# Performance work log

Hardware: AMD Instinct MI355X
Metric: run time of the kernel (lower is better)

Reference implementation:

```python
import jax, jax.numpy as jnp
import numpy as np

SR = 22050
N_MELS = 128
N_FFT = 2048
HOP = 512


def _mel_filterbank(sr, n_fft, n_mels):
    """librosa slaney-scale, slaney-normalized mel filterbank [n_mels, 1+n_fft//2]."""
    f_sp = 200.0 / 3
    min_log_hz = 1000.0
    min_log_mel = min_log_hz / f_sp
    logstep = np.log(6.4) / 27.0

    def hz_to_mel(f):
        f = np.asarray(f, dtype=np.float64)
        return np.where(f >= min_log_hz,
                        min_log_mel + np.log(np.maximum(f, min_log_hz) / min_log_hz) / logstep,
                        f / f_sp)

    def mel_to_hz(m):
        m = np.asarray(m, dtype=np.float64)
        return np.where(m >= min_log_mel,
                        min_log_hz * np.exp(logstep * (m - min_log_mel)),
                        f_sp * m)

    fmax = sr / 2.0
    fftfreqs = np.linspace(0.0, sr / 2.0, 1 + n_fft // 2)
    mel_f = mel_to_hz(np.linspace(hz_to_mel(0.0), hz_to_mel(fmax), n_mels + 2))
    fdiff = np.diff(mel_f)
    ramps = mel_f[:, None] - fftfreqs[None, :]
    lower = -ramps[:-2] / fdiff[:-1, None]
    upper = ramps[2:] / fdiff[1:, None]
    weights = np.maximum(0.0, np.minimum(lower, upper))
    enorm = 2.0 / (mel_f[2:n_mels + 2] - mel_f[:n_mels])  # slaney norm
    weights *= enorm[:, None]
    return weights.astype(np.float32)


def setup_inputs() -> dict:
    key = jax.random.key(0)
    x = jax.random.normal(key, (8, 661500, 2), dtype=jnp.float32) * 0.1
    mel_fb = jnp.asarray(_mel_filterbank(SR, N_FFT, N_MELS))  # [n_mels, 1+n_fft//2]
    return {"x": x, "mel_fb": mel_fb}


def reference(x, mel_fb):
    # x: (B, S, C) -> (B, n_mels, T, C), power-2 mel spectrogram (librosa defaults)
    y = jnp.transpose(x, (0, 2, 1))  # (B, C, S)
    pad = N_FFT // 2
    y = jnp.pad(y, ((0, 0), (0, 0), (pad, pad)), mode='reflect')
    n_frames = 1 + (y.shape[-1] - N_FFT) // HOP
    n = jnp.arange(N_FFT)
    # periodic hann window (scipy get_window('hann', N, fftbins=True))
    window = (0.5 - 0.5 * jnp.cos(2.0 * jnp.pi * n / N_FFT)).astype(x.dtype)
    idx = jnp.arange(n_frames)[:, None] * HOP + n[None, :]  # (T, n_fft)
    frames = y[:, :, idx] * window  # (B, C, T, n_fft)
    spec = jnp.fft.rfft(frames, axis=-1)  # (B, C, T, 1+n_fft//2)
    power = spec.real ** 2 + spec.imag ** 2  # |STFT|^2
    mel = jnp.einsum('mf,bctf->bmtc', mel_fb, power)  # (B, n_mels, T, C)
    return mel
```

## Files before the change

### kernel.cpp

```cpp
#include <hip/hip_runtime.h>
#include <math.h>

#define N_MELS   128
#define N_FFT    2048
#define HOP      512
#define BATCH    8
#define S_LEN    661500
#define CH       2
#define T_FRAMES 1292
#define NBINS    1025

#define ANG 0.003067961575771282f

#define WS_WIN     0
#define WS_TW      8192
#define WS_WBEG    24576
#define WS_WTAB    25600

#define PW_OFF   1056
#define PW_FR    2112

#define ZN 2304

__device__ __forceinline__ float2 cadd(float2 a, float2 b){ return make_float2(a.x+b.x, a.y+b.y); }
__device__ __forceinline__ float2 csub(float2 a, float2 b){ return make_float2(a.x-b.x, a.y-b.y); }
__device__ __forceinline__ float2 cmul(float2 a, float2 b){ return make_float2(a.x*b.x - a.y*b.y, a.x*b.y + a.y*b.x); }
__device__ __forceinline__ float2 cnegi(float2 z){ return make_float2(z.y, -z.x); }

__device__ __forceinline__ void bfly8(const float2* a, float2* b) {
    const float C = 0.70710678118654752f;
    float2 e0=cadd(a[0],a[4]), e1=cadd(a[1],a[5]), e2=cadd(a[2],a[6]), e3=cadd(a[3],a[7]);
    float2 o0=csub(a[0],a[4]), o1=csub(a[1],a[5]), o2=csub(a[2],a[6]), o3=csub(a[3],a[7]);
    float2 t1 = make_float2(C*(o1.x+o1.y), C*(o1.y-o1.x));
    float2 t2 = make_float2(o2.y, -o2.x);
    float2 t3 = make_float2(C*(o3.y-o3.x), -C*(o3.x+o3.y));
    {
        float2 s0=cadd(e0,e2), d0=csub(e0,e2);
        float2 s1=cadd(e1,e3), d1=csub(e1,e3);
        b[0]=cadd(s0,s1); b[4]=csub(s0,s1);
        b[2]=cadd(d0,cnegi(d1)); b[6]=csub(d0,cnegi(d1));
    }
    {
        float2 s0=cadd(o0,t2), d0=csub(o0,t2);
        float2 s1=cadd(t1,t3), d1=csub(t1,t3);
        b[1]=cadd(s0,s1); b[5]=csub(s0,s1);
        b[3]=cadd(d0,cnegi(d1)); b[7]=csub(d0,cnegi(d1));
    }
}

__device__ __forceinline__ void stage_pair(float2* rA, float2* rB, float2 w1) {
    float2 bqA[8], bqB[8];
    bfly8(rA, bqA);
    bfly8(rB, bqB);
    rA[0] = bqA[0]; rB[0] = bqB[0];
    float2 wk = w1;
    #pragma unroll
    for (int k = 1; k < 8; ++k) {
        rA[k] = cmul(wk, bqA[k]);
        rB[k] = cmul(wk, bqB[k]);
        wk = cmul(wk, w1);
    }
}

__device__ __forceinline__ void bf4(const float2* I, float2* O) {
    float2 apc=cadd(I[0],I[2]), amc=csub(I[0],I[2]);
    float2 bpd=cadd(I[1],I[3]), bmd=csub(I[1],I[3]);
    O[0]=cadd(apc,bpd); O[1]=cadd(amc,cnegi(bmd));
    O[2]=csub(apc,bpd); O[3]=csub(amc,cnegi(bmd));
}

__device__ __forceinline__ float2 upair(float2 Zf, float2 Zm) {
    float br = Zm.x, bi = -Zm.y;
    float e0 = Zf.x + br, e1 = Zf.y + bi;
    float o0 = Zf.y - bi, o1 = Zf.x - br;
    return make_float2(0.25f*(e0*e0 + e1*e1), 0.25f*(o0*o0 + o1*o1));
}

__global__ __launch_bounds__(256) void setup_kernel(
        const float* __restrict__ fb, float* __restrict__ ws) {
    int blk = blockIdx.x;
    if (blk < 8) {
        int i = blk * 256 + threadIdx.x;
        float*  win = ws;
        float2* tw  = (float2*)((char*)ws + WS_TW);
        win[i] = 0.5f - 0.5f * cosf(ANG * (float)i);
        float sn, cs; sincosf(-ANG * (float)i, &sn, &cs);
        tw[i] = make_float2(cs, sn);
    } else {
        int m = blk - 8;
        int lane = threadIdx.x;
        if (lane < 64) {
            int*   wbeg = (int*)((char*)ws + WS_WBEG);
            float* wtab = (float*)((char*)ws + WS_WTAB);
            const float* row = fb + m * NBINS;
            int s = NBINS;
            for (int f = lane; f < NBINS; f += 64)
                if (row[f] != 0.0f && f < s) s = f;
            #pragma unroll
            for (int o = 32; o; o >>= 1) s = min(s, __shfl_xor(s, o));
            int a0 = s & ~3;
            if (a0 > NBINS - 1) a0 = (NBINS - 1) & ~3;
            if (lane == 0) wbeg[m] = a0;
            int f = a0 + lane;
            wtab[(m << 6) + lane] = (f < NBINS) ? row[f] : 0.0f;
        }
    }
}

__global__ __launch_bounds__(256, 4) void mel_spec_kernel(
        const float* __restrict__ x, const float* __restrict__ fb,
        const float* __restrict__ ws, float* __restrict__ out) {
    __shared__ float4 Zq[ZN/2];
    float2* Z2  = (float2*)Zq;
    float*  pwb = (float*)Zq;

    const float*  win  = ws;
    const float2* tw   = (const float2*)((const char*)ws + WS_TW);
    const int*    wbeg = (const int*)((const char*)ws + WS_WBEG);
    const float*  wtab = (const float*)((const char*)ws + WS_WTAB);

    const int tid = threadIdx.x;
    const int bid = blockIdx.x;
    const int b   = bid & 7;
    const int t0  = (bid >> 3) * 2;

    const float2* xb = (const float2*)x + (size_t)b * S_LEN;
    const int tbA = t0*HOP - (N_FFT/2);
    const int tbB = tbA + HOP;

    float2 rA[8], rB[8];
    const int rb = tid + 2*(tid>>4);

    if (tbA >= 0 && tbB + (N_FFT - 1) < S_LEN) {
        #pragma unroll
        for (int k = 0; k < 8; ++k) {
            int n = tid + 256*k;
            float w = win[n];
            float2 vA = xb[tbA + n];
            float2 vB = xb[tbB + n];
            rA[k] = make_float2(vA.x*w, vA.y*w);
            rB[k] = make_float2(vB.x*w, vB.y*w);
        }
    } else {
        #pragma unroll
        for (int k = 0; k < 8; ++k) {
            int n  = tid + 256*k;
            float w = win[n];
            int sA = tbA + n;
            if (sA < 0) sA = -sA; else if (sA >= S_LEN) sA = 2*S_LEN - 2 - sA;
            float2 vA = xb[sA];
            rA[k] = make_float2(vA.x*w, vA.y*w);
            int sB = tbB + n;
            if (sB < 0) sB = -sB; else if (sB >= S_LEN) sB = 2*S_LEN - 2 - sB;
            float2 vB = xb[sB];
            rB[k] = make_float2(vB.x*w, vB.y*w);
        }
    }

    stage_pair(rA, rB, tw[tid]);
    {
        const int f4 = 4*tid + (tid>>1);
        #pragma unroll
        for (int j = 0; j < 4; ++j)
            Zq[f4+j] = make_float4(rA[2*j].x, rA[2*j].y, rA[2*j+1].x, rA[2*j+1].y);
        __syncthreads();
        #pragma unroll
        for (int k = 0; k < 8; ++k) rA[k] = Z2[rb + 288*k];
        __syncthreads();
        #pragma unroll
        for (int j = 0; j < 4; ++j)
            Zq[f4+j] = make_float4(rB[2*j].x, rB[2*j].y, rB[2*j+1].x, rB[2*j+1].y);
        __syncthreads();
        #pragma unroll
        for (int k = 0; k < 8; ++k) rB[k] = Z2[rb + 288*k];
        __syncthreads();
    }

    stage_pair(rA, rB, tw[tid & ~7]);
    {
        const int base = (tid & 7) + 72*(tid >> 3);
        #pragma unroll
        for (int k = 0; k < 8; ++k) Z2[base + 8*k + 2*(k>>1)] = rA[k];
        __syncthreads();
        #pragma unroll
        for (int k = 0; k < 8; ++k) rA[k] = Z2[rb + 288*k];
        __syncthreads();
        #pragma unroll
        for (int k = 0; k < 8; ++k) Z2[base + 8*k + 2*(k>>1)] = rB[k];
        __syncthreads();
        #pragma unroll
        for (int k = 0; k < 8; ++k) rB[k] = Z2[rb + 288*k];
        __syncthreads();
    }

    stage_pair(rA, rB, tw[tid & ~63]);
    const int b2  = (tid == 0) ? 256 : 512 - tid;
    const int rb2 = b2 + 2*(b2>>4);
    float2 A1[4], A2[4], B1[4], B2[4];
    {
        const int q = tid & 63;
        const int base = q + 2*(q>>4) + 576*(tid >> 6);
        #pragma unroll
        for (int k = 0; k < 8; ++k) Z2[base + 72*k] = rA[k];
        __syncthreads();
        #pragma unroll
        for (int k = 0; k < 4; ++k) { A1[k] = Z2[rb + 576*k]; A2[k] = Z2[rb2 + 576*k]; }
        __syncthreads();
        #pragma unroll
        for (int k = 0; k < 8; ++k) Z2[base + 72*k] = rB[k];
        __syncthreads();
        #pragma unroll
        for (int k = 0; k < 4; ++k) { B1[k] = Z2[rb + 576*k]; B2[k] = Z2[rb2 + 576*k]; }
        __syncthreads();
    }

    {
        float2 O1[4], O2[4];
        bf4(A1, O1); bf4(A2, O2);
        float* pwf = pwb;
        if (tid == 0) {
            float2 p;
            p = upair(O1[0], O1[0]); pwf[0]    = p.x; pwf[PW_OFF+0]    = p.y;
            p = upair(O1[1], O1[3]); pwf[512]  = p.x; pwf[PW_OFF+512]  = p.y;
            p = upair(O1[2], O1[2]); pwf[1024] = p.x; pwf[PW_OFF+1024] = p.y;
            p = upair(O2[0], O2[3]); pwf[256]  = p.x; pwf[PW_OFF+256]  = p.y;
            p = upair(O2[1], O2[2]); pwf[768]  = p.x; pwf[PW_OFF+768]  = p.y;
        } else {
            float2 p;
            p = upair(O1[0], O2[3]); pwf[tid]      = p.x; pwf[PW_OFF+tid]      = p.y;
            p = upair(O1[1], O2[2]); pwf[tid+512]  = p.x; pwf[PW_OFF+tid+512]  = p.y;
            p = upair(O2[0], O1[3]); pwf[512-tid]  = p.x; pwf[PW_OFF+512-tid]  = p.y;
            p = upair(O2[1], O1[2]); pwf[1024-tid] = p.x; pwf[PW_OFF+1024-tid] = p.y;
        }
    }
    {
        float2 O1[4], O2[4];
        bf4(B1, O1); bf4(B2, O2);
        float* pwf = pwb + PW_FR;
        if (tid == 0) {
            float2 p;
            p = upair(O1[0], O1[0]); pwf[0]    = p.x; pwf[PW_OFF+0]    = p.y;
            p = upair(O1[1], O1[3]); pwf[512]  = p.x; pwf[PW_OFF+512]  = p.y;
            p = upair(O1[2], O1[2]); pwf[1024] = p.x; pwf[PW_OFF+1024] = p.y;
            p = upair(O2[0], O2[3]); pwf[256]  = p.x; pwf[PW_OFF+256]  = p.y;
            p = upair(O2[1], O2[2]); pwf[768]  = p.x; pwf[PW_OFF+768]  = p.y;
        } else {
            float2 p;
            p = upair(O1[0], O2[3]); pwf[tid]      = p.x; pwf[PW_OFF+tid]      = p.y;
            p = upair(O1[1], O2[2]); pwf[tid+512]  = p.x; pwf[PW_OFF+tid+512]  = p.y;
            p = upair(O2[0], O1[3]); pwf[512-tid]  = p.x; pwf[PW_OFF+512-tid]  = p.y;
            p = upair(O2[1], O1[2]); pwf[1024-tid] = p.x; pwf[PW_OFF+1024-tid] = p.y;
        }
    }
    __syncthreads();

    {
        int m = tid >> 1;
        int h = tid & 1;
        int a0 = wbeg[m];
        const float4* wt4 = (const float4*)(wtab + (m << 6));
        const float*  p0  = pwb + h*PW_FR + a0;
        const float*  p1  = pwb + h*PW_FR + PW_OFF + a0;
        float acc0 = 0.0f, acc1 = 0.0f;
        #pragma unroll
        for (int j = 0; j < 16; ++j) {
            float4 w4 = wt4[j];
            float4 q0 = *(const float4*)(p0 + 4*j);
            float4 q1 = *(const float4*)(p1 + 4*j);
            acc0 += w4.x*q0.x + w4.y*q0.y + w4.z*q0.z + w4.w*q0.w;
            acc1 += w4.x*q1.x + w4.y*q1.y + w4.z*q1.z + w4.w*q1.w;
        }
        size_t base = (((size_t)b * N_MELS + m) * T_FRAMES + t0 + h) * CH;
        *(float2*)(out + base) = make_float2(acc0, acc1);
    }
}

extern "C" void kernel_launch(void* const* d_in, const int* in_sizes, int n_in,
                              void* d_out, int out_size, void* d_ws, size_t ws_size,
                              hipStream_t stream) {
    const float* x  = (const float*)d_in[0];
    const float* fb = (const float*)d_in[1];
    float* out = (float*)d_out;
    float* ws  = (float*)d_ws;

    setup_kernel<<<8 + N_MELS, 256, 0, stream>>>(fb, ws);
    mel_spec_kernel<<<BATCH * (T_FRAMES/2), 256, 0, stream>>>(x, fb, ws, out);
}
```

Before: 120.7 us.

## Process four frames per block with shared overlapping input and dual LDS buffers

Each block now computes four STFT frames instead of two. It loads one contiguous 3584-sample span once and reuses the overlapping windows across frames, instead of loading each frame separately. Two LDS buffers let the two paired FFTs transpose together, which halves the number of barriers per pair. The mel reduction reuses each weight load across four frames. The cost is double the shared memory, higher register pressure (14 input samples, four held power arrays), fewer blocks, and explicit zeroing of the padded tail of the power buffer.

```diff
diff --git a/kernel.cpp b/kernel.cpp
--- a/kernel.cpp
+++ b/kernel.cpp
@@ -17,8 +17,8 @@
 #define WS_WBEG    24576
 #define WS_WTAB    25600
 
-#define PW_OFF   1056
-#define PW_FR    2112
+#define PW_OFF   1060
+#define PW_FR    2120
 
 #define ZN 2304
 
@@ -74,6 +74,97 @@
     float e0 = Zf.x + br, e1 = Zf.y + bi;
     float o0 = Zf.y - bi, o1 = Zf.x - br;
     return make_float2(0.25f*(e0*e0 + e1*e1), 0.25f*(o0*o0 + o1*o1));
+}
+
+__device__ __forceinline__ void fft2048_pair(
+        float2* rA, float2* rB, float4* Zq0, float4* Zq1,
+        const float2* tw, int tid, int rb, int rb2,
+        float2* A1, float2* A2, float2* B1, float2* B2)
+{
+    float2* Z0 = (float2*)Zq0;
+    float2* Z1 = (float2*)Zq1;
+
+    stage_pair(rA, rB, tw[tid]);
+    {
+        const int f4 = 4*tid + (tid>>1);
+        #pragma unroll
+        for (int j = 0; j < 4; ++j) {
+            Zq0[f4+j] = make_float4(rA[2*j].x, rA[2*j].y, rA[2*j+1].x, rA[2*j+1].y);
+            Zq1[f4+j] = make_float4(rB[2*j].x, rB[2*j].y, rB[2*j+1].x, rB[2*j+1].y);
+        }
+        __syncthreads();
+        #pragma unroll
+        for (int k = 0; k < 8; ++k) { rA[k] = Z0[rb + 288*k]; rB[k] = Z1[rb + 288*k]; }
+        __syncthreads();
+    }
+
+    stage_pair(rA, rB, tw[tid & ~7]);
+    {
+        const int base = (tid & 7) + 72*(tid >> 3);
+        #pragma unroll
+        for (int k = 0; k < 8; ++k) {
+            Z0[base + 8*k + 2*(k>>1)] = rA[k];
+            Z1[base + 8*k + 2*(k>>1)] = rB[k];
+        }
+        __syncthreads();
+        #pragma unroll
+        for (int k = 0; k < 8; ++k) { rA[k] = Z0[rb + 288*k]; rB[k] = Z1[rb + 288*k]; }
+        __syncthreads();
+    }
+
+    stage_pair(rA, rB, tw[tid & ~63]);
+    {
+        const int q = tid & 63;
+        const int base = q + 2*(q>>4) + 576*(tid >> 6);
+        #pragma unroll
+        for (int k = 0; k < 8; ++k) {
+            Z0[base + 72*k] = rA[k];
+            Z1[base + 72*k] = rB[k];
+        }
+        __syncthreads();
+        #pragma unroll
+        for (int k = 0; k < 4; ++k) {
+            A1[k] = Z0[rb + 576*k]; A2[k] = Z0[rb2 + 576*k];
+            B1[k] = Z1[rb + 576*k]; B2[k] = Z1[rb2 + 576*k];
+        }
+        __syncthreads();
+    }
+}
+
+__device__ __forceinline__ void finish_frame(const float2* F1, const float2* F2,
+                                             int tid, float2* p)
+{
+    float2 O1[4], O2[4];
+    bf4(F1, O1); bf4(F2, O2);
+    if (tid == 0) {
+        p[0] = upair(O1[0], O1[0]);
+        p[1] = upair(O1[1], O1[3]);
+        p[2] = upair(O1[2], O1[2]);
+        p[3] = upair(O2[0], O2[3]);
+        p[4] = upair(O2[1], O2[2]);
+    } else {
+        p[0] = upair(O1[0], O2[3]);
+        p[1] = upair(O1[1], O2[2]);
+        p[2] = upair(O2[0], O1[3]);
+        p[3] = upair(O2[1], O1[2]);
+        p[4] = make_float2(0.0f, 0.0f);
+    }
+}
+
+__device__ __forceinline__ void store_frame(float* pwf, int tid, const float2* p)
+{
+    if (tid == 0) {
+        pwf[0]    = p[0].x; pwf[PW_OFF+0]    = p[0].y;
+        pwf[512]  = p[1].x; pwf[PW_OFF+512]  = p[1].y;
+        pwf[1024] = p[2].x; pwf[PW_OFF+1024] = p[2].y;
+        pwf[256]  = p[3].x; pwf[PW_OFF+256]  = p[3].y;
+        pwf[768]  = p[4].x; pwf[PW_OFF+768]  = p[4].y;
+    } else {
+        pwf[tid]      = p[0].x; pwf[PW_OFF+tid]      = p[0].y;
+        pwf[tid+512]  = p[1].x; pwf[PW_OFF+tid+512]  = p[1].y;
+        pwf[512-tid]  = p[2].x; pwf[PW_OFF+512-tid]  = p[2].y;
+        pwf[1024-tid] = p[3].x; pwf[PW_OFF+1024-tid] = p[3].y;
+    }
 }
 
 __global__ __launch_bounds__(256) void setup_kernel(
@@ -110,8 +201,9 @@
 __global__ __launch_bounds__(256, 4) void mel_spec_kernel(
         const float* __restrict__ x, const float* __restrict__ fb,
         const float* __restrict__ ws, float* __restrict__ out) {
-    __shared__ float4 Zq[ZN/2];
-    float2* Z2  = (float2*)Zq;
+    __shared__ float4 Zq[ZN];
+    float4* Zq0 = Zq;
+    float4* Zq1 = Zq + (ZN/2);
     float*  pwb = (float*)Zq;
 
     const float*  win  = ws;
@@ -122,156 +214,92 @@
     const int tid = threadIdx.x;
     const int bid = blockIdx.x;
     const int b   = bid & 7;
-    const int t0  = (bid >> 3) * 2;
+    const int t0  = (bid >> 3) * 4;
 
     const float2* xb = (const float2*)x + (size_t)b * S_LEN;
-    const int tbA = t0*HOP - (N_FFT/2);
-    const int tbB = tbA + HOP;
-
-    float2 rA[8], rB[8];
-    const int rb = tid + 2*(tid>>4);
-
-    if (tbA >= 0 && tbB + (N_FFT - 1) < S_LEN) {
-        #pragma unroll
-        for (int k = 0; k < 8; ++k) {
-            int n = tid + 256*k;
-            float w = win[n];
-            float2 vA = xb[tbA + n];
-            float2 vB = xb[tbB + n];
-            rA[k] = make_float2(vA.x*w, vA.y*w);
-            rB[k] = make_float2(vB.x*w, vB.y*w);
-        }
-    } else {
-        #pragma unroll
-        for (int k = 0; k < 8; ++k) {
-            int n  = tid + 256*k;
-            float w = win[n];
-            int sA = tbA + n;
-            if (sA < 0) sA = -sA; else if (sA >= S_LEN) sA = 2*S_LEN - 2 - sA;
-            float2 vA = xb[sA];
-            rA[k] = make_float2(vA.x*w, vA.y*w);
-            int sB = tbB + n;
-            if (sB < 0) sB = -sB; else if (sB >= S_LEN) sB = 2*S_LEN - 2 - sB;
-            float2 vB = xb[sB];
-            rB[k] = make_float2(vB.x*w, vB.y*w);
-        }
-    }
-
-    stage_pair(rA, rB, tw[tid]);
-    {
-        const int f4 = 4*tid + (tid>>1);
-        #pragma unroll
-        for (int j = 0; j < 4; ++j)
-            Zq[f4+j] = make_float4(rA[2*j].x, rA[2*j].y, rA[2*j+1].x, rA[2*j+1].y);
-        __syncthreads();
-        #pragma unroll
-        for (int k = 0; k < 8; ++k) rA[k] = Z2[rb + 288*k];
-        __syncthreads();
-        #pragma unroll
-        for (int j = 0; j < 4; ++j)
-            Zq[f4+j] = make_float4(rB[2*j].x, rB[2*j].y, rB[2*j+1].x, rB[2*j+1].y);
-        __syncthreads();
-        #pragma unroll
-        for (int k = 0; k < 8; ++k) rB[k] = Z2[rb + 288*k];
-        __syncthreads();
-    }
-
-    stage_pair(rA, rB, tw[tid & ~7]);
-    {
-        const int base = (tid & 7) + 72*(tid >> 3);
-        #pragma unroll
-        for (int k = 0; k < 8; ++k) Z2[base + 8*k + 2*(k>>1)] = rA[k];
-        __syncthreads();
-        #pragma unroll
-        for (int k = 0; k < 8; ++k) rA[k] = Z2[rb + 288*k];
-        __syncthreads();
-        #pragma unroll
-        for (int k = 0; k < 8; ++k) Z2[base + 8*k + 2*(k>>1)] = rB[k];
-        __syncthreads();
-        #pragma unroll
-        for (int k = 0; k < 8; ++k) rB[k] = Z2[rb + 288*k];
-        __syncthreads();
-    }
-
-    stage_pair(rA, rB, tw[tid & ~63]);
+    const int tb0 = t0*HOP - (N_FFT/2);
+
+    const int rb  = tid + 2*(tid>>4);
     const int b2  = (tid == 0) ? 256 : 512 - tid;
     const int rb2 = b2 + 2*(b2>>4);
+
+    float2 v[14];
+    float  wv[8];
+    if (tb0 >= 0 && tb0 + (3584 - 1) < S_LEN) {
+        #pragma unroll
+        for (int k = 0; k < 14; ++k) v[k] = xb[tb0 + tid + 256*k];
+    } else {
+        #pragma unroll
+        for (int k = 0; k < 14; ++k) {
+            int s = tb0 + tid + 256*k;
+            if (s < 0) s = -s; else if (s >= S_LEN) s = 2*S_LEN - 2 - s;
+            v[k] = xb[s];
+        }
+    }
+    #pragma unroll
+    for (int k = 0; k < 8; ++k) wv[k] = win[tid + 256*k];
+
+    float2 rA[8], rB[8];
     float2 A1[4], A2[4], B1[4], B2[4];
-    {
-        const int q = tid & 63;
-        const int base = q + 2*(q>>4) + 576*(tid >> 6);
-        #pragma unroll
-        for (int k = 0; k < 8; ++k) Z2[base + 72*k] = rA[k];
-        __syncthreads();
-        #pragma unroll
-        for (int k = 0; k < 4; ++k) { A1[k] = Z2[rb + 576*k]; A2[k] = Z2[rb2 + 576*k]; }
-        __syncthreads();
-        #pragma unroll
-        for (int k = 0; k < 8; ++k) Z2[base + 72*k] = rB[k];
-        __syncthreads();
-        #pragma unroll
-        for (int k = 0; k < 4; ++k) { B1[k] = Z2[rb + 576*k]; B2[k] = Z2[rb2 + 576*k]; }
-        __syncthreads();
-    }
-
-    {
-        float2 O1[4], O2[4];
-        bf4(A1, O1); bf4(A2, O2);
-        float* pwf = pwb;
-        if (tid == 0) {
-            float2 p;
-            p = upair(O1[0], O1[0]); pwf[0]    = p.x; pwf[PW_OFF+0]    = p.y;
-            p = upair(O1[1], O1[3]); pwf[512]  = p.x; pwf[PW_OFF+512]  = p.y;
-            p = upair(O1[2], O1[2]); pwf[1024] = p.x; pwf[PW_OFF+1024] = p.y;
-            p = upair(O2[0], O2[3]); pwf[256]  = p.x; pwf[PW_OFF+256]  = p.y;
-            p = upair(O2[1], O2[2]); pwf[768]  = p.x; pwf[PW_OFF+768]  = p.y;
-        } else {
-            float2 p;
-            p = upair(O1[0], O2[3]); pwf[tid]      = p.x; pwf[PW_OFF+tid]      = p.y;
-            p = upair(O1[1], O2[2]); pwf[tid+512]  = p.x; pwf[PW_OFF+tid+512]  = p.y;
-            p = upair(O2[0], O1[3]); pwf[512-tid]  = p.x; pwf[PW_OFF+512-tid]  = p.y;
-            p = upair(O2[1], O1[2]); pwf[1024-tid] = p.x; pwf[PW_OFF+1024-tid] = p.y;
-        }
-    }
-    {
-        float2 O1[4], O2[4];
-        bf4(B1, O1); bf4(B2, O2);
-        float* pwf = pwb + PW_FR;
-        if (tid == 0) {
-            float2 p;
-            p = upair(O1[0], O1[0]); pwf[0]    = p.x; pwf[PW_OFF+0]    = p.y;
-            p = upair(O1[1], O1[3]); pwf[512]  = p.x; pwf[PW_OFF+512]  = p.y;
-            p = upair(O1[2], O1[2]); pwf[1024] = p.x; pwf[PW_OFF+1024] = p.y;
-            p = upair(O2[0], O2[3]); pwf[256]  = p.x; pwf[PW_OFF+256]  = p.y;
-            p = upair(O2[1], O2[2]); pwf[768]  = p.x; pwf[PW_OFF+768]  = p.y;
-        } else {
-            float2 p;
-            p = upair(O1[0], O2[3]); pwf[tid]      = p.x; pwf[PW_OFF+tid]      = p.y;
-            p = upair(O1[1], O2[2]); pwf[tid+512]  = p.x; pwf[PW_OFF+tid+512]  = p.y;
-            p = upair(O2[0], O1[3]); pwf[512-tid]  = p.x; pwf[PW_OFF+512-tid]  = p.y;
-            p = upair(O2[1], O1[2]); pwf[1024-tid] = p.x; pwf[PW_OFF+1024-tid] = p.y;
-        }
+    float2 pA[5], pB[5], pC[5], pD[5];
+
+    #pragma unroll
+    for (int k = 0; k < 8; ++k) {
+        rA[k] = make_float2(v[k].x*wv[k],   v[k].y*wv[k]);
+        rB[k] = make_float2(v[k+2].x*wv[k], v[k+2].y*wv[k]);
+    }
+    fft2048_pair(rA, rB, Zq0, Zq1, tw, tid, rb, rb2, A1, A2, B1, B2);
+    finish_frame(A1, A2, tid, pA);
+    finish_frame(B1, B2, tid, pB);
+
+    #pragma unroll
+    for (int k = 0; k < 8; ++k) {
+        rA[k] = make_float2(v[k+4].x*wv[k], v[k+4].y*wv[k]);
+        rB[k] = make_float2(v[k+6].x*wv[k], v[k+6].y*wv[k]);
+    }
+    fft2048_pair(rA, rB, Zq0, Zq1, tw, tid, rb, rb2, A1, A2, B1, B2);
+    finish_frame(A1, A2, tid, pC);
+    finish_frame(B1, B2, tid, pD);
+
+    store_frame(pwb + 0*PW_FR, tid, pA);
+    store_frame(pwb + 1*PW_FR, tid, pB);
+    store_frame(pwb + 2*PW_FR, tid, pC);
+    store_frame(pwb + 3*PW_FR, tid, pD);
+    {
+        int i = tid;
+        int pl = i / 35, o = i - pl*35;
+        if (i < 280) pwb[(pl>>1)*PW_FR + (pl&1)*PW_OFF + 1025 + o] = 0.0f;
+        i = tid + 256;
+        pl = i / 35; o = i - pl*35;
+        if (i < 280) pwb[(pl>>1)*PW_FR + (pl&1)*PW_OFF + 1025 + o] = 0.0f;
     }
     __syncthreads();
 
     {
-        int m = tid >> 1;
-        int h = tid & 1;
+        int m  = tid >> 1;
+        int h0 = tid & 1;
         int a0 = wbeg[m];
         const float4* wt4 = (const float4*)(wtab + (m << 6));
-        const float*  p0  = pwb + h*PW_FR + a0;
-        const float*  p1  = pwb + h*PW_FR + PW_OFF + a0;
-        float acc0 = 0.0f, acc1 = 0.0f;
+        const float*  q00 = pwb +  h0   *PW_FR + a0;
+        const float*  q01 = pwb +  h0   *PW_FR + PW_OFF + a0;
+        const float*  q10 = pwb + (h0+2)*PW_FR + a0;
+        const float*  q11 = pwb + (h0+2)*PW_FR + PW_OFF + a0;
+        float a00 = 0.0f, a01 = 0.0f, a10 = 0.0f, a11 = 0.0f;
         #pragma unroll
         for (int j = 0; j < 16; ++j) {
             float4 w4 = wt4[j];
-            float4 q0 = *(const float4*)(p0 + 4*j);
-            float4 q1 = *(const float4*)(p1 + 4*j);
-            acc0 += w4.x*q0.x + w4.y*q0.y + w4.z*q0.z + w4.w*q0.w;
-            acc1 += w4.x*q1.x + w4.y*q1.y + w4.z*q1.z + w4.w*q1.w;
-        }
-        size_t base = (((size_t)b * N_MELS + m) * T_FRAMES + t0 + h) * CH;
-        *(float2*)(out + base) = make_float2(acc0, acc1);
+            float4 r0 = *(const float4*)(q00 + 4*j);
+            float4 r1 = *(const float4*)(q01 + 4*j);
+            float4 r2 = *(const float4*)(q10 + 4*j);
+            float4 r3 = *(const float4*)(q11 + 4*j);
+            a00 += w4.x*r0.x + w4.y*r0.y + w4.z*r0.z + w4.w*r0.w;
+            a01 += w4.x*r1.x + w4.y*r1.y + w4.z*r1.z + w4.w*r1.w;
+            a10 += w4.x*r2.x + w4.y*r2.y + w4.z*r2.z + w4.w*r2.w;
+            a11 += w4.x*r3.x + w4.y*r3.y + w4.z*r3.z + w4.w*r3.w;
+        }
+        size_t base = (((size_t)b * N_MELS + m) * T_FRAMES + t0 + h0) * CH;
+        *(float2*)(out + base)         = make_float2(a00, a01);
+        *(float2*)(out + base + 2*CH)  = make_float2(a10, a11);
     }
 }
 
@@ -284,5 +312,5 @@
     float* ws  = (float*)d_ws;
 
     setup_kernel<<<8 + N_MELS, 256, 0, stream>>>(fb, ws);
-    mel_spec_kernel<<<BATCH * (T_FRAMES/2), 256, 0, stream>>>(x, fb, ws, out);
-}
+    mel_spec_kernel<<<BATCH * (T_FRAMES/4), 256, 0, stream>>>(x, fb, ws, out);
+}
```

Result: slower. 132.8 us (+10.0%).
